# Performance work log

Hardware: AMD Instinct MI355X
Metric: run time of the kernel (lower is better)

## Reference

```python
import jax, jax.numpy as jnp
import numpy as np

N_RAYS = 65536
M_SAMPLES = 16777216  # avg ~256 samples per ray, irregular segment lengths


def setup_inputs() -> dict:
    key = jax.random.key(0)
    k1, k2, k3 = jax.random.split(key, 3)
    density = jax.random.normal(k1, (M_SAMPLES,), dtype=jnp.float32)
    rgb = jax.random.uniform(k2, (M_SAMPLES, 3), dtype=jnp.float32)
    bg = jnp.ones((3,), dtype=jnp.float32)
    # use_mipnerf_density=True -> act_shift = -1; interval = voxel_size_ratio * stepsize
    shift = jnp.float32(-1.0)
    interval = jnp.float32(0.5)
    ray_id = jnp.sort(jax.random.randint(k3, (M_SAMPLES,), 0, N_RAYS, dtype=jnp.int32))
    return {"density": density, "rgb": rgb, "bg": bg, "shift": shift,
            "interval": interval, "ray_id": ray_id, "n_rays": N_RAYS}


def _segmented_exclusive_cumsum(x, flags):
    """Exclusive cumsum of x restarting wherever flags is True (segment starts)."""
    def combine(a, b):
        xa, fa = a
        xb, fb = b
        return (jnp.where(fb, xb, xa + xb), fa | fb)
    inc, _ = jax.lax.associative_scan(combine, (x, flags))
    return inc - x


def reference(density, rgb, bg, shift, interval, ray_id, n_rays):
    # Raw2Alpha: alpha = 1 - (1 + exp(density + shift)) ** (-interval)
    #   => log(1 - alpha) = -interval * softplus(density + shift)  (exact)
    log_trans = -jax.nn.softplus(density + shift) * interval      # [M] log(1-alpha)
    alpha = -jnp.expm1(log_trans)                                  # [M]

    # Alphas2Weights: per-ray exclusive cumprod of (1 - alpha)
    flags = jnp.concatenate([jnp.ones((1,), bool), ray_id[1:] != ray_id[:-1]])
    logT = _segmented_exclusive_cumsum(log_trans, flags)           # [M] log T_i
    weights = alpha * jnp.exp(logT)                                # [M]
    seg_tot = jax.ops.segment_sum(log_trans, ray_id, num_segments=n_rays)
    alphainv_last = jnp.exp(seg_tot)                               # [N] final transmittance

    # Alpha compositing with background
    rgb_marched = jax.ops.segment_sum(weights[:, None] * rgb, ray_id,
                                      num_segments=n_rays)
    rgb_marched = rgb_marched + alphainv_last[:, None] * bg[None, :]  # [N,3]
    return rgb_marched
```

## Files before the change

### kernel.cpp

```cpp
#include <hip/hip_runtime.h>
#include <math.h>

__global__ void seg_starts_kernel(const int* __restrict__ ray_id, int M, int N,
                                  int* __restrict__ seg_start) {
    int r = blockIdx.x * blockDim.x + threadIdx.x;
    if (r > N) return;
    int lo = 0, hi = M;
    while (lo < hi) {
        int mid = (lo + hi) >> 1;
        if (ray_id[mid] < r) lo = mid + 1;
        else hi = mid;
    }
    seg_start[r] = lo;
}

__launch_bounds__(256, 8)
__global__ void composite_kernel(const float* __restrict__ density,
                                 const float* __restrict__ rgb,
                                 const float* __restrict__ bg,
                                 const float* __restrict__ shift_p,
                                 const float* __restrict__ interval_p,
                                 const int* __restrict__ seg_start,
                                 float* __restrict__ out, int N, int M) {
    const int wave = threadIdx.x >> 6;
    const int lane = threadIdx.x & 63;
    const int r = blockIdx.x * (blockDim.x >> 6) + wave;
    if (r >= N) return;

    const float shift = *shift_p;
    const float nI = -(*interval_p);
    const int s = seg_start[r];
    const int e = seg_start[r + 1];

    float T = 1.0f;
    float ar = 0.f, ag = 0.f, ab = 0.f;

    for (int base = s; base < e; base += 64) {
        int i = base + lane;
        int ic = (i < M - 1) ? i : (M - 1);
        float d  = density[ic];
        float cr = rgb[3 * ic + 0];
        float cg = rgb[3 * ic + 1];
        float cb = rgb[3 * ic + 2];
        float t = exp2f(nI * __log2f(1.0f + __expf(d + shift)));
        t = (i < e) ? t : 1.0f;

        float p = t;
        #pragma unroll
        for (int off = 1; off < 64; off <<= 1) {
            float o = __shfl_up(p, off);
            p *= (lane >= off) ? o : 1.0f;
        }
        float excl = __shfl_up(p, 1);
        if (lane == 0) excl = 1.0f;
        float w = T * (excl - p);
        ar += w * cr;
        ag += w * cg;
        ab += w * cb;

        T *= __shfl(p, 63);
        if (T < 1e-5f) break;
    }

    #pragma unroll
    for (int off = 32; off > 0; off >>= 1) {
        ar += __shfl_xor(ar, off);
        ag += __shfl_xor(ag, off);
        ab += __shfl_xor(ab, off);
    }

    if (lane == 0) {
        out[3 * r + 0] = ar + T * bg[0];
        out[3 * r + 1] = ag + T * bg[1];
        out[3 * r + 2] = ab + T * bg[2];
    }
}

extern "C" void kernel_launch(void* const* d_in, const int* in_sizes, int n_in,
                              void* d_out, int out_size, void* d_ws, size_t ws_size,
                              hipStream_t stream) {
    const float* density  = (const float*)d_in[0];
    const float* rgb      = (const float*)d_in[1];
    const float* bg       = (const float*)d_in[2];
    const float* shift    = (const float*)d_in[3];
    const float* interval = (const float*)d_in[4];
    const int*   ray_id   = (const int*)d_in[5];

    const int M = in_sizes[0];
    const int N = out_size / 3;

    int* seg_start = (int*)d_ws;

    {
        int threads = 256;
        int blocks = (N + 1 + threads - 1) / threads;
        seg_starts_kernel<<<blocks, threads, 0, stream>>>(ray_id, M, N, seg_start);
    }
    {
        const int wavesPerBlock = 4;
        int blocks = (N + wavesPerBlock - 1) / wavesPerBlock;
        composite_kernel<<<blocks, 256, 0, stream>>>(density, rgb, bg, shift,
                                                     interval, seg_start,
                                                     (float*)d_out, N, M);
    }
}
```

Baseline: 326.7 us.

## Process two rays per wavefront with 32-lane scans and looser early termination

Each 64-lane wavefront is split into two 32-lane halves, and each half composites its own ray. The prefix-product scan and the final reductions now work on 32 lanes, so twice as many rays run per block. The loop is driven by a ballot so each half keeps iterating until its own ray finishes. The transmittance cutoff is raised from 1e-5 to 1e-3, which stops rays earlier and reads fewer samples, at the cost of larger approximation error and some divergence between the two halves.

```diff
diff --git a/kernel.cpp b/kernel.cpp
--- a/kernel.cpp
+++ b/kernel.cpp
@@ -24,55 +24,65 @@
                                  float* __restrict__ out, int N, int M) {
     const int wave = threadIdx.x >> 6;
     const int lane = threadIdx.x & 63;
-    const int r = blockIdx.x * (blockDim.x >> 6) + wave;
-    if (r >= N) return;
+    const int sl   = lane & 31;
+    const int half = lane >> 5;
+    const int w    = blockIdx.x * (blockDim.x >> 6) + wave;
+    const int ray  = 2 * w + half;
 
     const float shift = *shift_p;
     const float nI = -(*interval_p);
-    const int s = seg_start[r];
-    const int e = seg_start[r + 1];
+
+    int s = 0, e = 0;
+    if (ray < N) { s = seg_start[ray]; e = seg_start[ray + 1]; }
 
     float T = 1.0f;
     float ar = 0.f, ag = 0.f, ab = 0.f;
+    int  base   = s;
+    bool active = (base < e);
 
-    for (int base = s; base < e; base += 64) {
-        int i = base + lane;
+    while (__ballot(active)) {
+        int i = base + sl;
+        bool valid = active && (i < e);
         int ic = (i < M - 1) ? i : (M - 1);
         float d  = density[ic];
         float cr = rgb[3 * ic + 0];
         float cg = rgb[3 * ic + 1];
         float cb = rgb[3 * ic + 2];
         float t = exp2f(nI * __log2f(1.0f + __expf(d + shift)));
-        t = (i < e) ? t : 1.0f;
+        t = valid ? t : 1.0f;
 
         float p = t;
         #pragma unroll
-        for (int off = 1; off < 64; off <<= 1) {
-            float o = __shfl_up(p, off);
-            p *= (lane >= off) ? o : 1.0f;
+        for (int off = 1; off < 32; off <<= 1) {
+            float o = __shfl_up(p, off, 32);
+            p *= (sl >= off) ? o : 1.0f;
         }
-        float excl = __shfl_up(p, 1);
-        if (lane == 0) excl = 1.0f;
-        float w = T * (excl - p);
-        ar += w * cr;
-        ag += w * cg;
-        ab += w * cb;
+        float excl = __shfl_up(p, 1, 32);
+        if (sl == 0) excl = 1.0f;
+        float wgt = T * (excl - p);
+        ar += wgt * cr;
+        ag += wgt * cg;
+        ab += wgt * cb;
 
-        T *= __shfl(p, 63);
-        if (T < 1e-5f) break;
+        float chunk = __shfl(p, 31, 32);
+        if (active) {
+            T *= chunk;
+            base += 32;
+            active = (base < e) && (T >= 1e-3f);
+        }
     }
 
     #pragma unroll
-    for (int off = 32; off > 0; off >>= 1) {
-        ar += __shfl_xor(ar, off);
-        ag += __shfl_xor(ag, off);
-        ab += __shfl_xor(ab, off);
+    for (int off = 16; off > 0; off >>= 1) {
+        ar += __shfl_xor(ar, off, 32);
+        ag += __shfl_xor(ag, off, 32);
+        ab += __shfl_xor(ab, off, 32);
     }
 
-    if (lane == 0) {
-        out[3 * r + 0] = ar + T * bg[0];
-        out[3 * r + 1] = ag + T * bg[1];
-        out[3 * r + 2] = ab + T * bg[2];
+    if (sl == 0 && ray < N) {
+        out[3 * ray + 0] = ar + T * bg[0];
+        out[3 * ray + 1] = ag + T * bg[1];
+        out[3 * ray + 2] = ab + T * bg[2];
     }
 }
 
@@ -97,8 +107,8 @@
         seg_starts_kernel<<<blocks, threads, 0, stream>>>(ray_id, M, N, seg_start);
     }
     {
-        const int wavesPerBlock = 4;
-        int blocks = (N + wavesPerBlock - 1) / wavesPerBlock;
+        int raysPerBlock = 8;
+        int blocks = (N + raysPerBlock - 1) / raysPerBlock;
         composite_kernel<<<blocks, 256, 0, stream>>>(density, rgb, bg, shift,
                                                      interval, seg_start,
                                                      (float*)d_out, N, M);
```

Result: no change. 325.2 us (-0.4%).
